# Kernel optimization log

Hardware: AMD Instinct MI355X
Metric: run time of the kernel (lower is better)

Reference implementation:

```python
import jax, jax.numpy as jnp
import numpy as np

K = 5          # number of neighbors (topk k=5+1, drop self)
EPS = 1e-05    # hparams['epsilon'] for gentropy term


def setup_inputs() -> dict:
    key = jax.random.key(0)
    k1, k2, k3, k4, k5 = jax.random.split(key, 5)
    B, D, C, N = 256, 256, 64, 200000
    features = jax.random.normal(k1, (B, D), dtype=jnp.float32)
    W = jax.random.normal(k2, (D, C), dtype=jnp.float32) * 0.05
    b = jnp.zeros((C,), dtype=jnp.float32)
    fea_bank = jax.random.normal(k3, (N, D), dtype=jnp.float32)
    # score bank holds softmax outputs -> make rows valid probability distributions
    score_bank = jax.nn.softmax(jax.random.normal(k4, (N, C), dtype=jnp.float32), axis=-1)
    trg_idx = jax.random.randint(k5, (B,), 0, N, dtype=jnp.int64)
    return {"features": features, "W": W, "b": b,
            "fea_bank": fea_bank, "score_bank": score_bank, "trg_idx": trg_idx}


def reference(features, W, b, fea_bank, score_bank, trg_idx):
    sg = jax.lax.stop_gradient
    B = features.shape[0]
    C = W.shape[1]

    logits = features @ W + b                       # classifier(features)
    softmax_out = jax.nn.softmax(logits, axis=-1)   # [B, C] (differentiable)

    # --- everything bank-related is under torch.no_grad in the original ---
    nrm = jnp.maximum(jnp.linalg.norm(features, axis=1, keepdims=True), 1e-12)
    f_norm = sg(features / nrm)                     # F.normalize(features)
    fb = sg(fea_bank.at[trg_idx].set(f_norm))        # fea_bank[trg_idx] = f_norm
    sb = sg(score_bank.at[trg_idx].set(sg(softmax_out)))

    dist = f_norm @ fb.T                             # [B, N]
    _, idx_near = jax.lax.top_k(dist, K + 1)
    idx_near = idx_near[:, 1:]                       # [B, K] drop self

    score_near = sb[idx_near]                        # [B, K, C]
    fea_near = fb[idx_near]                          # [B, K, D]

    dist2 = jnp.einsum('bkd,nd->bkn', fea_near, fb)  # [B, K, N]
    _, idx_nn = jax.lax.top_k(dist2, K + 1)
    idx_nn = idx_nn[:, :, 1:]                        # [B, K, K]

    match = (idx_nn == trg_idx[:, None, None]).sum(-1).astype(jnp.float32)  # [B, K]
    weight = jnp.where(match > 0.0, match, jnp.float32(0.1))                # [B, K]
    weight_kk = jnp.full((B, K * K), 0.1, dtype=jnp.float32)  # fill_(0.1) overwrites

    score_near_kk = sb[idx_nn].reshape(B, K * K, C)  # [B, K*K, C]
    # --- end no_grad region ---

    # F.kl_div(input, target, reduction='none') = target * (log(target) - input)
    # (original passes probabilities, not log-probs, as input -- kept faithfully)
    kl_kk = score_near_kk * (jnp.log(score_near_kk) - softmax_out[:, None, :])
    loss = jnp.mean((kl_kk.sum(-1) * weight_kk).sum(1))

    kl_n = score_near * (jnp.log(score_near) - softmax_out[:, None, :])
    loss = loss + jnp.mean((kl_n.sum(-1) * weight).sum(1))

    msoftmax = softmax_out.mean(axis=0)
    gentropy = jnp.sum(msoftmax * jnp.log(msoftmax + EPS))
    loss = loss + gentropy
    return loss
```

## Files before the change

kernel.cpp:

```cpp
#include <hip/hip_runtime.h>
#include <hip/hip_bf16.h>
#include <math.h>

#define B_SZ   256
#define D_DIM  256
#define C_DIM  64
#define N_CAND 200000
#define K_TOP  5
#define CH32   32
#define CH32_SH 8192
#define QTILE_SH 16384
#define NCH32  (N_CAND / CH32)
#define NCHJ1  16
#define NCHJ2  32
#define S1     ((NCH32 + NCHJ1 - 1) / NCHJ1)
#define S2     ((NCH32 + NCHJ2 - 1) / NCHJ2)

typedef short bf16x8 __attribute__((ext_vector_type(8)));
typedef float f32x16 __attribute__((ext_vector_type(16)));
typedef unsigned short u16x8 __attribute__((ext_vector_type(8)));

__device__ __forceinline__ bool better(float v1, int i1, float v2, int i2) {
    return (v1 > v2) || (v1 == v2 && i1 < i2);
}

__device__ __forceinline__ void insert6f(float* lv, int* li, float v, int idx) {
    if (better(v, idx, lv[5], li[5])) {
        lv[5] = v; li[5] = idx;
        #pragma unroll
        for (int k = 5; k > 0; --k) {
            if (better(lv[k], li[k], lv[k - 1], li[k - 1])) {
                float tv = lv[k]; lv[k] = lv[k - 1]; lv[k - 1] = tv;
                int   ti = li[k]; li[k] = li[k - 1]; li[k - 1] = ti;
            }
        }
    }
}

__device__ __forceinline__ void merge6(const float* av, const int* ai,
                                       const float* bv, const int* bi,
                                       float* ov, int* oi) {
    int ia = 0, ib = 0;
    #pragma unroll
    for (int k = 0; k < 6; ++k) {
        bool ta;
        if (ia >= 6)      ta = false;
        else if (ib >= 6) ta = true;
        else              ta = better(av[ia], ai[ia], bv[ib], bi[ib]);
        if (ta) { ov[k] = av[ia]; oi[k] = ai[ia]; ++ia; }
        else    { ov[k] = bv[ib]; oi[k] = bi[ib]; ++ib; }
    }
}

__device__ __forceinline__ unsigned med3u(unsigned a, unsigned b, unsigned c) {
    unsigned d;
    asm("v_med3_u32 %0, %1, %2, %3" : "=v"(d) : "v"(a), "v"(b), "v"(c));
    return d;
}

__device__ __forceinline__ void kinsert(unsigned* kv, unsigned x) {
    unsigned n0 = kv[0] > x ? kv[0] : x;
    unsigned n1 = med3u(x, kv[0], kv[1]);
    unsigned n2 = med3u(x, kv[1], kv[2]);
    unsigned n3 = med3u(x, kv[2], kv[3]);
    unsigned n4 = med3u(x, kv[3], kv[4]);
    unsigned n5 = med3u(x, kv[4], kv[5]);
    kv[0] = n0; kv[1] = n1; kv[2] = n2; kv[3] = n3; kv[4] = n4; kv[5] = n5;
}

__device__ __forceinline__ unsigned short bf16rne(float x) {
    unsigned int u = __float_as_uint(x);
    unsigned int r = u + 0x7fffu + ((u >> 16) & 1u);
    return (unsigned short)(r >> 16);
}

__device__ __forceinline__ u16x8 pack8(float4 a, float4 b) {
    u16x8 h;
    h[0] = bf16rne(a.x); h[1] = bf16rne(a.y); h[2] = bf16rne(a.z); h[3] = bf16rne(a.w);
    h[4] = bf16rne(b.x); h[5] = bf16rne(b.y); h[6] = bf16rne(b.z); h[7] = bf16rne(b.w);
    return h;
}

__global__ void k_init(int* pos_of, float* accp) {
    int i = blockIdx.x * 256 + threadIdx.x;
    if (i < N_CAND) pos_of[i] = -1;
    if (i == 0) accp[0] = 0.f;
}

__global__ void k_scatter(const int* __restrict__ trg, int* __restrict__ pos_of) {
    int j = threadIdx.x;
    atomicMax(&pos_of[trg[j]], j);
}

__global__ __launch_bounds__(256) void k_prep(const float* __restrict__ features,
                                              const float* __restrict__ W,
                                              const float* __restrict__ bias,
                                              float* __restrict__ f_norm,
                                              float* __restrict__ softm) {
    int b = blockIdx.x, t = threadIdx.x;
    __shared__ float row[256];
    __shared__ float red[256];
    float x = features[b * D_DIM + t];
    row[t] = x; red[t] = x * x;
    __syncthreads();
    for (int s = 128; s > 0; s >>= 1) {
        if (t < s) red[t] += red[t + s];
        __syncthreads();
    }
    float nrm = fmaxf(sqrtf(red[0]), 1e-12f);
    f_norm[b * D_DIM + t] = x / nrm;
    if (t < C_DIM) {
        float acc = bias[t];
        for (int d = 0; d < D_DIM; ++d) acc = fmaf(row[d], W[d * C_DIM + t], acc);
        float mx = acc;
        for (int off = 32; off > 0; off >>= 1) mx = fmaxf(mx, __shfl_xor(mx, off, 64));
        float e = expf(acc - mx);
        float ssum = e;
        for (int off = 32; off > 0; off >>= 1) ssum += __shfl_xor(ssum, off, 64);
        softm[b * C_DIM + t] = e / ssum;
    }
}

__global__ __launch_bounds__(256) void k_convert(const float* __restrict__ fea_bank,
                                                 const float* __restrict__ f_norm,
                                                 const int* __restrict__ pos_of,
                                                 short* __restrict__ bank) {
    int cc = blockIdx.x, t = threadIdx.x;
    int r = t >> 2, q4 = t & 3;
    int n = cc * 64 + r;
    int p = pos_of[n];
    const float* src = (p >= 0) ? (f_norm + (size_t)p * D_DIM)
                                : (fea_bank + (size_t)n * D_DIM);
    short* dst = bank + (size_t)(cc * 2 + (r >> 5)) * CH32_SH;
    int rl = r & 31;
    #pragma unroll
    for (int i = 0; i < 8; ++i) {
        int kk = q4 * 64 + i * 8;
        float4 a = *(const float4*)(src + kk);
        float4 b = *(const float4*)(src + kk + 4);
        int e = ((kk >> 4) * 64) + (((kk >> 3) & 1) * 32) + rl;
        *(u16x8*)(dst + (size_t)e * 8) = pack8(a, b);
    }
}

__global__ __launch_bounds__(256) void k_permq(const float* __restrict__ rows,
                                               const float* __restrict__ fea_bank,
                                               const int* __restrict__ idx,
                                               const int* __restrict__ pos_of,
                                               short* __restrict__ dst) {
    int tile = blockIdx.x, t = threadIdx.x;
    int r = t >> 2, q4 = t & 3;
    const float* src;
    if (idx) {
        int n = idx[tile * 64 + r];
        int p = pos_of[n];
        src = (p >= 0) ? (rows + (size_t)p * D_DIM) : (fea_bank + (size_t)n * D_DIM);
    } else {
        src = rows + (size_t)(tile * 64 + r) * D_DIM;
    }
    short* d = dst + (size_t)tile * QTILE_SH;
    #pragma unroll
    for (int i = 0; i < 8; ++i) {
        int kk = q4 * 64 + i * 8;
        float4 a = *(const float4*)(src + kk);
        float4 b = *(const float4*)(src + kk + 4);
        int e = ((kk >> 4) * 128) + ((r >> 5) * 64) + (((kk >> 3) & 1) * 32) + (r & 31);
        *(u16x8*)(d + (size_t)e * 8) = pack8(a, b);
    }
}

__global__ __launch_bounds__(256, 4) void dist_topk(const short* __restrict__ qbf,
                                                    const short* __restrict__ bank,
                                                    float* __restrict__ pval,
                                                    int* __restrict__ pidx,
                                                    int nqt, int swz,
                                                    int S, int nchj) {
    __shared__ __align__(16) short sbuf[2 * CH32_SH];

    int slab, qt;
    if (swz) {
        int bid = blockIdx.x;
        int xcd = bid & 7;
        int rem = bid >> 3;
        qt = rem % nqt;
        slab = (rem / nqt) * 8 + xcd;
        if (slab >= S) return;
    } else {
        slab = blockIdx.x;
        qt = blockIdx.y;
    }
    const int cfirst = slab * nchj;
    int nch = NCH32 - cfirst; if (nch > nchj) nch = nchj;

    const int t   = threadIdx.x;
    const int w   = t >> 6;
    const int l   = t & 63;
    const int khv = l >> 5;
    const int col = l & 31;

    const short* qtile = qbf + (size_t)(qt * 2 + (w >> 1)) * QTILE_SH;
    const int half = w & 1;
    bf16x8 bfr[16];
    #pragma unroll
    for (int ks = 0; ks < 16; ++ks)
        bfr[ks] = *(const bf16x8*)(qtile + (size_t)(ks * 128 + half * 64 + l) * 8);

    unsigned kv[6];
    #pragma unroll
    for (int k = 0; k < 6; ++k) kv[k] = 0u;

    const short* sbase = bank + (size_t)cfirst * CH32_SH;

    #pragma unroll
    for (int i = 0; i < 4; ++i) {
        const short* gp = sbase + (size_t)(i * 256 + t) * 8;
        short* lp = sbuf + (size_t)(i * 256 + w * 64) * 8;
        __builtin_amdgcn_global_load_lds(
            (const __attribute__((address_space(1))) void*)gp,
            (__attribute__((address_space(3))) void*)lp, 16, 0, 0);
    }

    for (int ch = 0; ch < nch; ++ch) {
        const int cur = ch & 1;
        if (ch + 1 < nch) {
            const short* g = sbase + (size_t)(ch + 1) * CH32_SH;
            short* lbase = sbuf + (size_t)(cur ^ 1) * CH32_SH;
            #pragma unroll
            for (int i = 0; i < 4; ++i) {
                const short* gp = g + (size_t)(i * 256 + t) * 8;
                short* lp = lbase + (size_t)(i * 256 + w * 64) * 8;
                __builtin_amdgcn_global_load_lds(
                    (const __attribute__((address_space(1))) void*)gp,
                    (__attribute__((address_space(3))) void*)lp, 16, 0, 0);
            }
            asm volatile("s_waitcnt vmcnt(4)" ::: "memory");
        } else {
            asm volatile("s_waitcnt vmcnt(0)" ::: "memory");
        }
        __builtin_amdgcn_s_barrier();
        __builtin_amdgcn_sched_barrier(0);

        const short* cb = sbuf + (size_t)cur * CH32_SH;

        f32x16 a;
        #pragma unroll
        for (int i = 0; i < 16; ++i) a[i] = 2.0f;
        #pragma unroll
        for (int ks = 0; ks < 16; ++ks) {
            bf16x8 fa = *(const bf16x8*)(cb + (size_t)(ks * 64 + l) * 8);
            a = __builtin_amdgcn_mfma_f32_32x32x16_bf16(fa, bfr[ks], a, 0, 0, 0);
        }

        const unsigned invb = 1023u - (unsigned)(ch * 32);
        #pragma unroll
        for (int r = 0; r < 16; ++r) {
            unsigned m = (unsigned)((r & 3) + 8 * (r >> 2) + 4 * khv);
            unsigned x = (__float_as_uint(a[r]) & 0xFFFFFC00u) | (invb - m);
            kinsert(kv, x);
        }

        __builtin_amdgcn_sched_barrier(0);
        __builtin_amdgcn_s_barrier();
    }

    {
        int q = qt * 128 + w * 32 + col;
        size_t b0 = ((size_t)q * S + slab) * 12 + khv * 6;
        #pragma unroll
        for (int k = 0; k < 6; ++k) {
            unsigned key = kv[k];
            int pos = 1023 - (int)(key & 1023u);
            int c = pos >> 5, m = pos & 31;
            pval[b0 + k] = __uint_as_float(key & 0xFFFFFC00u);
            pidx[b0 + k] = (cfirst + c) * CH32 + m;
        }
    }
}

__global__ __launch_bounds__(256) void topk_merge(const float* __restrict__ pval,
                                                  const int* __restrict__ pidx,
                                                  int* __restrict__ out_idx,
                                                  int S) {
    int q = blockIdx.x, t = threadIdx.x;
    const int total = S * 12;
    float lv[6]; int li[6];
    #pragma unroll
    for (int k = 0; k < 6; ++k) { lv[k] = -3.4e38f; li[k] = 0x7fffffff; }
    size_t base = (size_t)q * total;
    for (int e = t; e < total; e += 256) insert6f(lv, li, pval[base + e], pidx[base + e]);
    __shared__ float sv[256][6];
    __shared__ int   si[256][6];
    #pragma unroll
    for (int k = 0; k < 6; ++k) { sv[t][k] = lv[k]; si[t][k] = li[k]; }
    __syncthreads();
    for (int w = 128; w >= 1; w >>= 1) {
        if (t < w) {
            float ov[6]; int oi[6];
            merge6(sv[t], si[t], sv[t + w], si[t + w], ov, oi);
            #pragma unroll
            for (int k = 0; k < 6; ++k) { sv[t][k] = ov[k]; si[t][k] = oi[k]; }
        }
        __syncthreads();
    }
    if (t == 0) {
        for (int k = 1; k < 6; ++k) out_idx[q * K_TOP + k - 1] = si[0][k];
    }
}

__global__ void k_loss(const float* __restrict__ softm, const float* __restrict__ score_bank,
                       const int* __restrict__ pos_of, const int* __restrict__ idx_near,
                       const int* __restrict__ idx_nn, const int* __restrict__ trg,
                       float* accp) {
    int b = blockIdx.x, c = threadIdx.x;
    float p_bc = softm[b * C_DIM + c];
    float part = 0.f;
    for (int k = 0; k < K_TOP; ++k) {
        for (int j = 0; j < K_TOP; ++j) {
            int n = idx_nn[(b * K_TOP + k) * K_TOP + j];
            int p = pos_of[n];
            const float* srow = (p >= 0) ? (softm + (size_t)p * C_DIM)
                                         : (score_bank + (size_t)n * C_DIM);
            float s = srow[c];
            float v = s * (logf(s) - p_bc);
            for (int off = 32; off > 0; off >>= 1) v += __shfl_down(v, off, 64);
            if (c == 0) part += 0.1f * v;
        }
    }
    for (int k = 0; k < K_TOP; ++k) {
        int n = idx_near[b * K_TOP + k];
        int p = pos_of[n];
        const float* srow = (p >= 0) ? (softm + (size_t)p * C_DIM)
                                     : (score_bank + (size_t)n * C_DIM);
        float s = srow[c];
        float v = s * (logf(s) - p_bc);
        for (int off = 32; off > 0; off >>= 1) v += __shfl_down(v, off, 64);
        if (c == 0) {
            int m = 0;
            for (int j = 0; j < K_TOP; ++j)
                m += (idx_nn[(b * K_TOP + k) * K_TOP + j] == trg[b]) ? 1 : 0;
            float w = (m > 0) ? (float)m : 0.1f;
            part += w * v;
        }
    }
    if (c == 0) atomicAdd(accp, part * (1.0f / (float)B_SZ));
}

__global__ void k_final(const float* __restrict__ softm, const float* __restrict__ accp,
                        float* __restrict__ out) {
    int c = threadIdx.x;
    float m = 0.f;
    for (int b = 0; b < B_SZ; ++b) m += softm[b * C_DIM + c];
    m *= (1.0f / (float)B_SZ);
    float g = m * logf(m + 1e-5f);
    for (int off = 32; off > 0; off >>= 1) g += __shfl_down(g, off, 64);
    if (c == 0) out[0] = accp[0] + g;
}

extern "C" void kernel_launch(void* const* d_in, const int* in_sizes, int n_in,
                              void* d_out, int out_size, void* d_ws, size_t ws_size,
                              hipStream_t stream) {
    const float* features   = (const float*)d_in[0];
    const float* W          = (const float*)d_in[1];
    const float* bias       = (const float*)d_in[2];
    const float* fea_bank   = (const float*)d_in[3];
    const float* score_bank = (const float*)d_in[4];
    const int*   trg        = (const int*)d_in[5];
    float* out = (float*)d_out;

    char* ws = (char*)d_ws;
    size_t off = 0;
    auto alloc = [&](size_t bytes) -> void* {
        void* p = ws + off;
        off = (off + bytes + 255) & ~(size_t)255;
        return p;
    };
    short* bankbf   = (short*)alloc((size_t)NCH32 * CH32_SH * 2);
    short* q1bf     = (short*)alloc((size_t)(B_SZ / 64) * QTILE_SH * 2);
    short* q2bf     = (short*)alloc((size_t)(B_SZ * K_TOP / 64) * QTILE_SH * 2);
    float* f_norm   = (float*)alloc((size_t)B_SZ * D_DIM * 4);
    float* softm    = (float*)alloc((size_t)B_SZ * C_DIM * 4);
    int*   pos_of   = (int*)alloc((size_t)N_CAND * 4);
    float* accp     = (float*)alloc(4);
    int*   idx_near = (int*)alloc((size_t)B_SZ * K_TOP * 4);
    int*   idx_nn   = (int*)alloc((size_t)B_SZ * K_TOP * K_TOP * 4);
    float* pv1      = (float*)alloc((size_t)B_SZ * S1 * 12 * 4);
    int*   pi1      = (int*)alloc((size_t)B_SZ * S1 * 12 * 4);
    float* pv2      = (float*)alloc((size_t)B_SZ * K_TOP * S2 * 12 * 4);
    int*   pi2      = (int*)alloc((size_t)B_SZ * K_TOP * S2 * 12 * 4);

    k_init<<<dim3((N_CAND + 255) / 256), dim3(256), 0, stream>>>(pos_of, accp);
    k_scatter<<<dim3(1), dim3(256), 0, stream>>>(trg, pos_of);
    k_prep<<<dim3(B_SZ), dim3(256), 0, stream>>>(features, W, bias, f_norm, softm);

    k_convert<<<dim3(NCH32 / 2), dim3(256), 0, stream>>>(fea_bank, f_norm, pos_of, bankbf);
    k_permq<<<dim3(B_SZ / 64), dim3(256), 0, stream>>>(f_norm, fea_bank, nullptr, pos_of, q1bf);

    dist_topk<<<dim3(S1, 2), dim3(256), 0, stream>>>(
        q1bf, bankbf, pv1, pi1, 2, 0, S1, NCHJ1);
    topk_merge<<<dim3(B_SZ), dim3(256), 0, stream>>>(pv1, pi1, idx_near, S1);

    k_permq<<<dim3(B_SZ * K_TOP / 64), dim3(256), 0, stream>>>(
        f_norm, fea_bank, idx_near, pos_of, q2bf);

    {
        int nqt = (B_SZ * K_TOP) / 128;
        int nsg = (S2 + 7) / 8;
        dist_topk<<<dim3(nsg * 8 * nqt), dim3(256), 0, stream>>>(
            q2bf, bankbf, pv2, pi2, nqt, 1, S2, NCHJ2);
    }
    topk_merge<<<dim3(B_SZ * K_TOP), dim3(256), 0, stream>>>(pv2, pi2, idx_nn, S2);

    k_loss<<<dim3(B_SZ), dim3(64), 0, stream>>>(softm, score_bank, pos_of, idx_near, idx_nn, trg, accp);
    k_final<<<dim3(1), dim3(64), 0, stream>>>(softm, accp, out);
}
```

Baseline: 331.9 us.

## Replace per-element top-k in MFMA loop with per-chunk max and rescoring

The distance kernel no longer keeps a running top-6 with med3 inserts over every score. It writes only the maximum score of each 32-candidate chunk. A new select kernel picks the top chunks by that maximum, keeps every chunk within a small tolerance of the sixth-best, and rescores those chunks' candidates exactly in bf16 to produce the final top-k. This removes the heavy per-element insert work from the hot loop, at the cost of a large cmax buffer write (N/32 floats per query), a global-memory rescoring pass, and a candidate cap (MAXC) that could drop true neighbours.

Measured after the change: 424.1 us. +27.8%, slower.

```diff
diff --git a/kernel.cpp b/kernel.cpp
--- a/kernel.cpp
+++ b/kernel.cpp
@@ -15,6 +15,7 @@
 #define NCHJ2  32
 #define S1     ((NCH32 + NCHJ1 - 1) / NCHJ1)
 #define S2     ((NCH32 + NCHJ2 - 1) / NCHJ2)
+#define MAXC   192
 
 typedef short bf16x8 __attribute__((ext_vector_type(8)));
 typedef float f32x16 __attribute__((ext_vector_type(16)));
@@ -52,26 +53,14 @@
     }
 }
 
-__device__ __forceinline__ unsigned med3u(unsigned a, unsigned b, unsigned c) {
-    unsigned d;
-    asm("v_med3_u32 %0, %1, %2, %3" : "=v"(d) : "v"(a), "v"(b), "v"(c));
-    return d;
-}
-
-__device__ __forceinline__ void kinsert(unsigned* kv, unsigned x) {
-    unsigned n0 = kv[0] > x ? kv[0] : x;
-    unsigned n1 = med3u(x, kv[0], kv[1]);
-    unsigned n2 = med3u(x, kv[1], kv[2]);
-    unsigned n3 = med3u(x, kv[2], kv[3]);
-    unsigned n4 = med3u(x, kv[3], kv[4]);
-    unsigned n5 = med3u(x, kv[4], kv[5]);
-    kv[0] = n0; kv[1] = n1; kv[2] = n2; kv[3] = n3; kv[4] = n4; kv[5] = n5;
-}
-
 __device__ __forceinline__ unsigned short bf16rne(float x) {
     unsigned int u = __float_as_uint(x);
     unsigned int r = u + 0x7fffu + ((u >> 16) & 1u);
     return (unsigned short)(r >> 16);
+}
+
+__device__ __forceinline__ float bf16f(unsigned short h) {
+    return __uint_as_float(((unsigned)h) << 16);
 }
 
 __device__ __forceinline__ u16x8 pack8(float4 a, float4 b) {
@@ -147,7 +136,8 @@
                                                const float* __restrict__ fea_bank,
                                                const int* __restrict__ idx,
                                                const int* __restrict__ pos_of,
-                                               short* __restrict__ dst) {
+                                               short* __restrict__ dst,
+                                               unsigned short* __restrict__ qplain) {
     int tile = blockIdx.x, t = threadIdx.x;
     int r = t >> 2, q4 = t & 3;
     const float* src;
@@ -159,22 +149,24 @@
         src = rows + (size_t)(tile * 64 + r) * D_DIM;
     }
     short* d = dst + (size_t)tile * QTILE_SH;
+    unsigned short* qp = qplain + (size_t)(tile * 64 + r) * D_DIM;
     #pragma unroll
     for (int i = 0; i < 8; ++i) {
         int kk = q4 * 64 + i * 8;
         float4 a = *(const float4*)(src + kk);
         float4 b = *(const float4*)(src + kk + 4);
+        u16x8 h = pack8(a, b);
         int e = ((kk >> 4) * 128) + ((r >> 5) * 64) + (((kk >> 3) & 1) * 32) + (r & 31);
-        *(u16x8*)(d + (size_t)e * 8) = pack8(a, b);
-    }
-}
-
-__global__ __launch_bounds__(256, 4) void dist_topk(const short* __restrict__ qbf,
-                                                    const short* __restrict__ bank,
-                                                    float* __restrict__ pval,
-                                                    int* __restrict__ pidx,
-                                                    int nqt, int swz,
-                                                    int S, int nchj) {
+        *(u16x8*)(d + (size_t)e * 8) = h;
+        *(u16x8*)(qp + kk) = h;
+    }
+}
+
+__global__ __launch_bounds__(256, 4) void dist_max(const short* __restrict__ qbf,
+                                                   const short* __restrict__ bank,
+                                                   float* __restrict__ cmax,
+                                                   int nqt, int swz,
+                                                   int S, int nchj) {
     __shared__ __align__(16) short sbuf[2 * CH32_SH];
 
     int slab, qt;
@@ -197,6 +189,7 @@
     const int l   = t & 63;
     const int khv = l >> 5;
     const int col = l & 31;
+    const int q   = qt * 128 + w * 32 + col;
 
     const short* qtile = qbf + (size_t)(qt * 2 + (w >> 1)) * QTILE_SH;
     const int half = w & 1;
@@ -204,10 +197,6 @@
     #pragma unroll
     for (int ks = 0; ks < 16; ++ks)
         bfr[ks] = *(const bf16x8*)(qtile + (size_t)(ks * 128 + half * 64 + l) * 8);
-
-    unsigned kv[6];
-    #pragma unroll
-    for (int k = 0; k < 6; ++k) kv[k] = 0u;
 
     const short* sbase = bank + (size_t)cfirst * CH32_SH;
 
@@ -220,6 +209,7 @@
             (__attribute__((address_space(3))) void*)lp, 16, 0, 0);
     }
 
+    float mxprev = 0.f;
     for (int ch = 0; ch < nch; ++ch) {
         const int cur = ch & 1;
         if (ch + 1 < nch) {
@@ -242,56 +232,96 @@
 
         const short* cb = sbuf + (size_t)cur * CH32_SH;
 
-        f32x16 a;
-        #pragma unroll
-        for (int i = 0; i < 16; ++i) a[i] = 2.0f;
+        f32x16 a = {};
         #pragma unroll
         for (int ks = 0; ks < 16; ++ks) {
             bf16x8 fa = *(const bf16x8*)(cb + (size_t)(ks * 64 + l) * 8);
             a = __builtin_amdgcn_mfma_f32_32x32x16_bf16(fa, bfr[ks], a, 0, 0, 0);
         }
 
-        const unsigned invb = 1023u - (unsigned)(ch * 32);
+        float mx = a[0];
         #pragma unroll
-        for (int r = 0; r < 16; ++r) {
-            unsigned m = (unsigned)((r & 3) + 8 * (r >> 2) + 4 * khv);
-            unsigned x = (__float_as_uint(a[r]) & 0xFFFFFC00u) | (invb - m);
-            kinsert(kv, x);
-        }
+        for (int r = 1; r < 16; ++r) mx = fmaxf(mx, a[r]);
+        mx = fmaxf(mx, __shfl_xor(mx, 32, 64));
+
+        if ((ch & 1) && khv == 0) {
+            float2 v = make_float2(mxprev, mx);
+            *(float2*)&cmax[(size_t)q * NCH32 + (cfirst + ch - 1)] = v;
+        }
+        mxprev = mx;
 
         __builtin_amdgcn_sched_barrier(0);
         __builtin_amdgcn_s_barrier();
     }
-
-    {
-        int q = qt * 128 + w * 32 + col;
-        size_t b0 = ((size_t)q * S + slab) * 12 + khv * 6;
-        #pragma unroll
-        for (int k = 0; k < 6; ++k) {
-            unsigned key = kv[k];
-            int pos = 1023 - (int)(key & 1023u);
-            int c = pos >> 5, m = pos & 31;
-            pval[b0 + k] = __uint_as_float(key & 0xFFFFFC00u);
-            pidx[b0 + k] = (cfirst + c) * CH32 + m;
-        }
-    }
-}
-
-__global__ __launch_bounds__(256) void topk_merge(const float* __restrict__ pval,
-                                                  const int* __restrict__ pidx,
-                                                  int* __restrict__ out_idx,
-                                                  int S) {
+}
+
+__global__ __launch_bounds__(256) void k_select(const float* __restrict__ cmax,
+                                                const unsigned short* __restrict__ qplain,
+                                                const float* __restrict__ fea_bank,
+                                                const float* __restrict__ f_norm,
+                                                const int* __restrict__ pos_of,
+                                                int* __restrict__ out_idx) {
     int q = blockIdx.x, t = threadIdx.x;
-    const int total = S * 12;
-    float lv[6]; int li[6];
-    #pragma unroll
-    for (int k = 0; k < 6; ++k) { lv[k] = -3.4e38f; li[k] = 0x7fffffff; }
-    size_t base = (size_t)q * total;
-    for (int e = t; e < total; e += 256) insert6f(lv, li, pval[base + e], pidx[base + e]);
     __shared__ float sv[256][6];
     __shared__ int   si[256][6];
+    __shared__ float qrow[256];
+    __shared__ int cnt;
+    __shared__ int list[MAXC];
+
+    const float* row = cmax + (size_t)q * NCH32;
+
+    float lv[6]; int li[6];
+    #pragma unroll
+    for (int k = 0; k < 6; ++k) { lv[k] = -3.4e38f; li[k] = 0x7fffffff; }
+    for (int c = t; c < NCH32; c += 256) insert6f(lv, li, row[c], c);
     #pragma unroll
     for (int k = 0; k < 6; ++k) { sv[t][k] = lv[k]; si[t][k] = li[k]; }
+    if (t == 0) cnt = 0;
+    __syncthreads();
+    for (int w = 128; w >= 1; w >>= 1) {
+        if (t < w) {
+            float ov[6]; int oi[6];
+            merge6(sv[t], si[t], sv[t + w], si[t + w], ov, oi);
+            #pragma unroll
+            for (int k = 0; k < 6; ++k) { sv[t][k] = ov[k]; si[t][k] = oi[k]; }
+        }
+        __syncthreads();
+    }
+    float tauM = sv[0][5] - 2e-4f;
+    __syncthreads();
+
+    for (int c = t; c < NCH32; c += 256) {
+        if (row[c] >= tauM) {
+            int k = atomicAdd(&cnt, 1);
+            if (k < MAXC) list[k] = c;
+        }
+    }
+    qrow[t] = bf16f(qplain[(size_t)q * D_DIM + t]);
+    __syncthreads();
+    int nc = cnt < MAXC ? cnt : MAXC;
+
+    float bv[6]; int bi[6];
+    #pragma unroll
+    for (int k = 0; k < 6; ++k) { bv[k] = -3.4e38f; bi[k] = 0x7fffffff; }
+    const int cand = t >> 3, d0 = (t & 7) * 32;
+    for (int ci = 0; ci < nc; ++ci) {
+        int c = list[ci];
+        int n = c * CH32 + cand;
+        int p = pos_of[n];
+        const float* src = (p >= 0) ? (f_norm + (size_t)p * D_DIM)
+                                    : (fea_bank + (size_t)n * D_DIM);
+        float acc = 0.f;
+        #pragma unroll
+        for (int d = 0; d < 32; ++d)
+            acc = fmaf(bf16f(bf16rne(src[d0 + d])), qrow[d0 + d], acc);
+        acc += __shfl_down(acc, 4, 8);
+        acc += __shfl_down(acc, 2, 8);
+        acc += __shfl_down(acc, 1, 8);
+        if ((t & 7) == 0) insert6f(bv, bi, acc, n);
+    }
+
+    #pragma unroll
+    for (int k = 0; k < 6; ++k) { sv[t][k] = bv[k]; si[t][k] = bi[k]; }
     __syncthreads();
     for (int w = 128; w >= 1; w >>= 1) {
         if (t < w) {
@@ -377,38 +407,41 @@
     short* bankbf   = (short*)alloc((size_t)NCH32 * CH32_SH * 2);
     short* q1bf     = (short*)alloc((size_t)(B_SZ / 64) * QTILE_SH * 2);
     short* q2bf     = (short*)alloc((size_t)(B_SZ * K_TOP / 64) * QTILE_SH * 2);
+    unsigned short* qplain1 = (unsigned short*)alloc((size_t)B_SZ * D_DIM * 2);
+    unsigned short* qplain2 = (unsigned short*)alloc((size_t)B_SZ * K_TOP * D_DIM * 2);
     float* f_norm   = (float*)alloc((size_t)B_SZ * D_DIM * 4);
     float* softm    = (float*)alloc((size_t)B_SZ * C_DIM * 4);
     int*   pos_of   = (int*)alloc((size_t)N_CAND * 4);
     float* accp     = (float*)alloc(4);
     int*   idx_near = (int*)alloc((size_t)B_SZ * K_TOP * 4);
     int*   idx_nn   = (int*)alloc((size_t)B_SZ * K_TOP * K_TOP * 4);
-    float* pv1      = (float*)alloc((size_t)B_SZ * S1 * 12 * 4);
-    int*   pi1      = (int*)alloc((size_t)B_SZ * S1 * 12 * 4);
-    float* pv2      = (float*)alloc((size_t)B_SZ * K_TOP * S2 * 12 * 4);
-    int*   pi2      = (int*)alloc((size_t)B_SZ * K_TOP * S2 * 12 * 4);
+    float* cmax1    = (float*)alloc((size_t)B_SZ * NCH32 * 4);
+    float* cmax2    = (float*)alloc((size_t)B_SZ * K_TOP * NCH32 * 4);
 
     k_init<<<dim3((N_CAND + 255) / 256), dim3(256), 0, stream>>>(pos_of, accp);
     k_scatter<<<dim3(1), dim3(256), 0, stream>>>(trg, pos_of);
     k_prep<<<dim3(B_SZ), dim3(256), 0, stream>>>(features, W, bias, f_norm, softm);
 
     k_convert<<<dim3(NCH32 / 2), dim3(256), 0, stream>>>(fea_bank, f_norm, pos_of, bankbf);
-    k_permq<<<dim3(B_SZ / 64), dim3(256), 0, stream>>>(f_norm, fea_bank, nullptr, pos_of, q1bf);
-
-    dist_topk<<<dim3(S1, 2), dim3(256), 0, stream>>>(
-        q1bf, bankbf, pv1, pi1, 2, 0, S1, NCHJ1);
-    topk_merge<<<dim3(B_SZ), dim3(256), 0, stream>>>(pv1, pi1, idx_near, S1);
+    k_permq<<<dim3(B_SZ / 64), dim3(256), 0, stream>>>(
+        f_norm, fea_bank, nullptr, pos_of, q1bf, qplain1);
+
+    dist_max<<<dim3(S1, 2), dim3(256), 0, stream>>>(
+        q1bf, bankbf, cmax1, 2, 0, S1, NCHJ1);
+    k_select<<<dim3(B_SZ), dim3(256), 0, stream>>>(
+        cmax1, qplain1, fea_bank, f_norm, pos_of, idx_near);
 
     k_permq<<<dim3(B_SZ * K_TOP / 64), dim3(256), 0, stream>>>(
-        f_norm, fea_bank, idx_near, pos_of, q2bf);
+        f_norm, fea_bank, idx_near, pos_of, q2bf, qplain2);
 
     {
         int nqt = (B_SZ * K_TOP) / 128;
         int nsg = (S2 + 7) / 8;
-        dist_topk<<<dim3(nsg * 8 * nqt), dim3(256), 0, stream>>>(
-            q2bf, bankbf, pv2, pi2, nqt, 1, S2, NCHJ2);
-    }
-    topk_merge<<<dim3(B_SZ * K_TOP), dim3(256), 0, stream>>>(pv2, pi2, idx_nn, S2);
+        dist_max<<<dim3(nsg * 8 * nqt), dim3(256), 0, stream>>>(
+            q2bf, bankbf, cmax2, nqt, 1, S2, NCHJ2);
+    }
+    k_select<<<dim3(B_SZ * K_TOP), dim3(256), 0, stream>>>(
+        cmax2, qplain2, fea_bank, f_norm, pos_of, idx_nn);
 
     k_loss<<<dim3(B_SZ), dim3(64), 0, stream>>>(softm, score_bank, pos_of, idx_near, idx_nn, trg, accp);
     k_final<<<dim3(1), dim3(64), 0, stream>>>(softm, accp, out);
```
